# Kernel tuning notes

Measured on AMD Instinct MI355X. Metric: run time of the kernel, lower is better.

## Reference

```python
import jax, jax.numpy as jnp
import numpy as np
import math

SCALE = 30.0
MARGIN = 0.5
THRESH = -math.cos(MARGIN)          # easy_margin=False branch
SIN_M = math.sin(MARGIN)
OUT_INDICATOR = 1.0

B, D, C = 256, 512, 100000


def setup_inputs() -> dict:
    key = jax.random.key(0)
    k1, k2, k3 = jax.random.split(key, 3)
    feat = jax.random.normal(k1, (B, D), dtype=jnp.float32)
    # xavier_uniform_ for [C, D] weight
    bound = math.sqrt(6.0 / (C + D))
    weights = jax.random.uniform(k2, (C, D), dtype=jnp.float32, minval=-bound, maxval=bound)
    label = jax.random.randint(k3, (B,), 0, C, dtype=jnp.int64)
    return {"feat": feat, "weights": weights, "label": label}


def reference(feat, weights, label):
    # L2-normalize features and class weights, then cosine logits  [B, C]
    nf = feat / jnp.linalg.norm(feat, axis=-1, keepdims=True)
    nw = weights / jnp.linalg.norm(weights, axis=-1, keepdims=True)
    cos = jnp.matmul(nf, nw.T)

    rows = jnp.arange(feat.shape[0])
    cos_target = cos[rows, label]                     # [B] cos(theta_yi)
    cond = cos_target > THRESH

    # vectorized equivalent of the per-row scatter loop
    margin_tables = jnp.zeros_like(cos).at[rows, label].add(
        jnp.where(cond, MARGIN, 0.0).astype(cos.dtype))
    margin_tables_ext = jnp.zeros_like(cos).at[rows, label].add(
        jnp.where(cond, 0.0, -MARGIN * SIN_M).astype(cos.dtype))
    margin_tables_ext = margin_tables_ext * OUT_INDICATOR

    marginal_logits = SCALE * (jnp.cos(jnp.arccos(cos) + margin_tables) + margin_tables_ext)
    return marginal_logits, SCALE * cos, weights
```

## Files before the change

### kernel.cpp

```cpp
#include <hip/hip_runtime.h>
#include <math.h>
#include <stdint.h>

typedef __attribute__((ext_vector_type(8))) short short8;
typedef __attribute__((ext_vector_type(4))) float f32x4;
typedef __attribute__((ext_vector_type(4))) unsigned int u32x4;

#define SCALE   30.0f
#define MARGIN  0.5f
#define COS_M   0.8775825618903728f
#define SIN_M   0.4794255386042030f
#define THRESH  (-0.8775825618903728f)

constexpr int Bsz = 256;
constexpr int Dd  = 512;
constexpr int Cc  = 100000;
constexpr int NT  = 782;
constexpr int KT  = 16;
constexpr int TILE_EL   = 4096;
constexpr int COMP_TILE = KT * TILE_EL;

__device__ __forceinline__ unsigned short f2bf(float x) {
    unsigned int u = __float_as_uint(x);
    u += 0x7fffu + ((u >> 16) & 1u);
    return (unsigned short)(u >> 16);
}
__device__ __forceinline__ float bf2f(unsigned short h) {
    return __uint_as_float(((unsigned int)h) << 16);
}

#define GLL16(gptr, lptr)                                                              \
    __builtin_amdgcn_global_load_lds(                                                  \
        (const __attribute__((address_space(1))) unsigned int*)(gptr),                 \
        (__attribute__((address_space(3))) unsigned int*)(lptr), 16, 0, 0)

__device__ __forceinline__ int swz_off(int rr, int ch) {
    return rr * 32 + ((ch ^ ((rr >> 1) & 3)) * 8);
}

__device__ __forceinline__ void split2(float a, float b, unsigned int& hp, unsigned int& lp) {
    unsigned short h0 = f2bf(a), h1 = f2bf(b);
    unsigned short l0 = f2bf(a - bf2f(h0));
    unsigned short l1 = f2bf(b - bf2f(h1));
    hp = (unsigned int)h0 | ((unsigned int)h1 << 16);
    lp = (unsigned int)l0 | ((unsigned int)l1 << 16);
}

__global__ __launch_bounds__(256) void prep_kernel(
    const float* __restrict__ W, const float* __restrict__ F,
    float* __restrict__ inv_w, float* __restrict__ w_copy,
    unsigned short* __restrict__ whM, unsigned short* __restrict__ wlM,
    unsigned short* __restrict__ whL, unsigned short* __restrict__ wlL,
    unsigned short* __restrict__ Ah,  unsigned short* __restrict__ Al)
{
    const int wid = threadIdx.x >> 6, lane = threadIdx.x & 63;
    const int tk = lane >> 2, ch = lane & 3;

    {
        int row = blockIdx.x * 4 + wid;
        const float* src = W + (size_t)row * Dd + lane * 8;
        f32x4 v0 = __builtin_nontemporal_load((const f32x4*)src);
        f32x4 v1 = __builtin_nontemporal_load((const f32x4*)src + 1);
        float v[8] = {v0.x, v0.y, v0.z, v0.w, v1.x, v1.y, v1.z, v1.w};

        float s = 0.f;
        #pragma unroll
        for (int p = 0; p < 8; ++p) s += v[p] * v[p];
        #pragma unroll
        for (int off = 32; off >= 1; off >>= 1) s += __shfl_xor(s, off, 64);
        if (lane == 0) inv_w[row] = 1.0f / sqrtf(s);

        if (w_copy) {
            f32x4* dst = (f32x4*)(w_copy + (size_t)row * Dd + lane * 8);
            __builtin_nontemporal_store(v0, dst);
            __builtin_nontemporal_store(v1, dst + 1);
        }

        unsigned int hp[4], lp[4];
        #pragma unroll
        for (int p = 0; p < 4; ++p) split2(v[2*p], v[2*p+1], hp[p], lp[p]);

        int tn = row >> 7, rr = row & 127;
        size_t off = (size_t)tk * TILE_EL + swz_off(rr, ch);
        unsigned short* ph = (tn == NT-1) ? whL : whM + (size_t)tn * COMP_TILE;
        unsigned short* pl = (tn == NT-1) ? wlL : wlM + (size_t)tn * COMP_TILE;
        *(u32x4*)(ph + off) = u32x4{hp[0], hp[1], hp[2], hp[3]};
        *(u32x4*)(pl + off) = u32x4{lp[0], lp[1], lp[2], lp[3]};
    }

    if (blockIdx.x < Bsz / 4) {
        int row = blockIdx.x * 4 + wid;
        const float* src = F + (size_t)row * Dd + lane * 8;
        f32x4 v0 = __builtin_nontemporal_load((const f32x4*)src);
        f32x4 v1 = __builtin_nontemporal_load((const f32x4*)src + 1);
        float v[8] = {v0.x, v0.y, v0.z, v0.w, v1.x, v1.y, v1.z, v1.w};

        float s = 0.f;
        #pragma unroll
        for (int p = 0; p < 8; ++p) s += v[p] * v[p];
        #pragma unroll
        for (int off = 32; off >= 1; off >>= 1) s += __shfl_xor(s, off, 64);
        float inv = 1.0f / sqrtf(s);

        unsigned int hp[4], lp[4];
        #pragma unroll
        for (int p = 0; p < 4; ++p) split2(v[2*p] * inv, v[2*p+1] * inv, hp[p], lp[p]);

        int tm = row >> 7, rr = row & 127;
        size_t off = ((size_t)(tm * KT + tk)) * TILE_EL + swz_off(rr, ch);
        *(u32x4*)(Ah + off) = u32x4{hp[0], hp[1], hp[2], hp[3]};
        *(u32x4*)(Al + off) = u32x4{lp[0], lp[1], lp[2], lp[3]};
    }
}

__global__ __launch_bounds__(256, 2) void gemm_kernel(
    const unsigned short* __restrict__ Ah, const unsigned short* __restrict__ Al,
    const unsigned short* __restrict__ WhM, const unsigned short* __restrict__ WlM,
    const unsigned short* __restrict__ WhL, const unsigned short* __restrict__ WlL,
    const float* __restrict__ inv_w, const int* __restrict__ label,
    float* __restrict__ out_ml, float* __restrict__ out_cos)
{
    __shared__ __align__(16) unsigned short Ash[TILE_EL];
    __shared__ __align__(16) unsigned short Asl[TILE_EL];
    __shared__ __align__(16) unsigned short Bsh[TILE_EL];
    __shared__ __align__(16) unsigned short Bsl[TILE_EL];

    int lin = blockIdx.x;
    int xcd = lin & 7, pos = lin >> 3;
    int swz = (xcd < 4 ? xcd * 196 : 784 + (xcd - 4) * 195) + pos;
    int tn = (NT - 1) - (swz >> 1);
    int tm = swz & 1;

    const int tid  = threadIdx.x;
    const int wid  = tid >> 6, lane = tid & 63;
    const int wm   = wid >> 1, wn   = wid & 1;
    const int lr   = lane & 15, lc  = lane >> 4;

    const unsigned short* ah0 = Ah + (size_t)tm * COMP_TILE;
    const unsigned short* al0 = Al + (size_t)tm * COMP_TILE;
    const unsigned short* bh0 = (tn == NT-1) ? WhL : WhM + (size_t)tn * COMP_TILE;
    const unsigned short* bl0 = (tn == NT-1) ? WlL : WlM + (size_t)tn * COMP_TILE;

    f32x4 acc[4][4];
    #pragma unroll
    for (int i = 0; i < 4; ++i)
        #pragma unroll
        for (int j = 0; j < 4; ++j)
            acc[i][j] = f32x4{0.f, 0.f, 0.f, 0.f};

    int aoff[4], boff[4];
    #pragma unroll
    for (int i = 0; i < 4; ++i) {
        aoff[i] = swz_off(wm * 64 + i * 16 + lr, lc);
        boff[i] = swz_off(wn * 64 + i * 16 + lr, lc);
    }

    for (int tk = 0; tk < KT; ++tk) {
        const unsigned short* ga  = ah0 + tk * TILE_EL;
        const unsigned short* gal = al0 + tk * TILE_EL;
        const unsigned short* gb  = bh0 + tk * TILE_EL;
        const unsigned short* gbl = bl0 + tk * TILE_EL;
        __syncthreads();
        GLL16(ga  + tid * 8,        &Ash[tid * 8]);
        GLL16(ga  + 2048 + tid * 8, &Ash[2048 + tid * 8]);
        GLL16(gal + tid * 8,        &Asl[tid * 8]);
        GLL16(gal + 2048 + tid * 8, &Asl[2048 + tid * 8]);
        GLL16(gb  + tid * 8,        &Bsh[tid * 8]);
        GLL16(gb  + 2048 + tid * 8, &Bsh[2048 + tid * 8]);
        GLL16(gbl + tid * 8,        &Bsl[tid * 8]);
        GLL16(gbl + 2048 + tid * 8, &Bsl[2048 + tid * 8]);
        __syncthreads();

        short8 fah[4], fal[4], fbh[4], fbl[4];
        #pragma unroll
        for (int i = 0; i < 4; ++i) {
            fah[i] = *(const short8*)&Ash[aoff[i]];
            fal[i] = *(const short8*)&Asl[aoff[i]];
            fbh[i] = *(const short8*)&Bsh[boff[i]];
            fbl[i] = *(const short8*)&Bsl[boff[i]];
        }
        #pragma unroll
        for (int i = 0; i < 4; ++i)
            #pragma unroll
            for (int j = 0; j < 4; ++j) {
                acc[i][j] = __builtin_amdgcn_mfma_f32_16x16x32_bf16(fah[i], fbh[j], acc[i][j], 0, 0, 0);
                acc[i][j] = __builtin_amdgcn_mfma_f32_16x16x32_bf16(fah[i], fbl[j], acc[i][j], 0, 0, 0);
                acc[i][j] = __builtin_amdgcn_mfma_f32_16x16x32_bf16(fal[i], fbh[j], acc[i][j], 0, 0, 0);
            }
    }

    const int n0  = tn * 128 + wn * 64;
    const int m0g = tm * 128 + wm * 64;
    float invw[4]; int ncol[4]; bool nok[4];
    #pragma unroll
    for (int j = 0; j < 4; ++j) {
        ncol[j] = n0 + j * 16 + lr;
        nok[j]  = (ncol[j] < Cc);
        invw[j] = nok[j] ? inv_w[ncol[j]] : 0.0f;
    }
    #pragma unroll
    for (int i = 0; i < 4; ++i) {
        #pragma unroll
        for (int r = 0; r < 4; ++r) {
            int m = m0g + i * 16 + lc * 4 + r;
            int lab = label[m];
            size_t base = (size_t)m * Cc;
            #pragma unroll
            for (int j = 0; j < 4; ++j) {
                float cosv = acc[i][j][r] * invw[j];
                float sc = SCALE * cosv;
                float ml = sc;
                if (ncol[j] == lab) {
                    if (cosv > THRESH) {
                        float sint = sqrtf(fmaxf(0.f, 1.f - cosv * cosv));
                        ml = SCALE * (cosv * COS_M - sint * SIN_M);
                    } else {
                        ml = SCALE * (cosv - MARGIN * SIN_M);
                    }
                }
                if (nok[j]) {
                    __builtin_nontemporal_store(ml, out_ml  + base + ncol[j]);
                    __builtin_nontemporal_store(sc, out_cos + base + ncol[j]);
                }
            }
        }
    }
}

extern "C" void kernel_launch(void* const* d_in, const int* in_sizes, int n_in,
                              void* d_out, int out_size, void* d_ws, size_t ws_size,
                              hipStream_t stream) {
    const float* feat  = (const float*)d_in[0];
    const float* W     = (const float*)d_in[1];
    const int*   label = (const int*)d_in[2];

    float* out     = (float*)d_out;
    float* out_ml  = out;
    float* out_cos = out + (size_t)Bsz * Cc;
    float* out_w   = out + (size_t)2 * Bsz * Cc;

    char* ws = (char*)d_ws;
    float* inv_w = (float*)ws;
    size_t off = (size_t)Cc * 4;
    unsigned short* Ah = (unsigned short*)(ws + off); off += (size_t)2 * COMP_TILE * 2;
    unsigned short* Al = (unsigned short*)(ws + off); off += (size_t)2 * COMP_TILE * 2;

    const size_t wsplit_bytes = (size_t)2 * NT * COMP_TILE * 2;
    bool big = ws_size >= off + wsplit_bytes;

    unsigned short *whM, *wlM, *whL, *wlL;
    float* w_copy;
    if (big) {
        whM = (unsigned short*)(ws + off);
        wlM = whM + (size_t)NT * COMP_TILE;
        whL = whM + (size_t)(NT - 1) * COMP_TILE;
        wlL = wlM + (size_t)(NT - 1) * COMP_TILE;
        w_copy = out_w;
    } else {
        whM = (unsigned short*)out_w;
        wlM = whM + (size_t)(NT - 1) * COMP_TILE;
        whL = (unsigned short*)(ws + off); off += (size_t)COMP_TILE * 2;
        wlL = (unsigned short*)(ws + off); off += (size_t)COMP_TILE * 2;
        w_copy = nullptr;
    }

    hipLaunchKernelGGL(prep_kernel, dim3(Cc / 4), dim3(256), 0, stream,
                       W, feat, inv_w, w_copy, whM, wlM, whL, wlL, Ah, Al);
    hipLaunchKernelGGL(gemm_kernel, dim3(2 * NT), dim3(256), 0, stream,
                       Ah, Al, whM, wlM, whL, wlL, inv_w, label, out_ml, out_cos);
    if (!big) {
        hipMemcpyAsync(out_w, W, (size_t)Cc * Dd * sizeof(float),
                       hipMemcpyDeviceToDevice, stream);
    }
}
```

Baseline: 628.8 us.

## Double-buffer LDS tiles to overlap global loads with MFMA compute

```diff
diff --git a/kernel.cpp b/kernel.cpp
--- a/kernel.cpp
+++ b/kernel.cpp
@@ -120,10 +120,10 @@
     const float* __restrict__ inv_w, const int* __restrict__ label,
     float* __restrict__ out_ml, float* __restrict__ out_cos)
 {
-    __shared__ __align__(16) unsigned short Ash[TILE_EL];
-    __shared__ __align__(16) unsigned short Asl[TILE_EL];
-    __shared__ __align__(16) unsigned short Bsh[TILE_EL];
-    __shared__ __align__(16) unsigned short Bsl[TILE_EL];
+    __shared__ __align__(16) unsigned short Ash[2][TILE_EL];
+    __shared__ __align__(16) unsigned short Asl[2][TILE_EL];
+    __shared__ __align__(16) unsigned short Bsh[2][TILE_EL];
+    __shared__ __align__(16) unsigned short Bsl[2][TILE_EL];
 
     int lin = blockIdx.x;
     int xcd = lin & 7, pos = lin >> 3;
@@ -155,29 +155,36 @@
         boff[i] = swz_off(wn * 64 + i * 16 + lr, lc);
     }
 
+    #define STAGE(c, t)                                                                \
+        do {                                                                           \
+            const unsigned short* ga_  = ah0 + (t) * TILE_EL;                          \
+            const unsigned short* gal_ = al0 + (t) * TILE_EL;                          \
+            const unsigned short* gb_  = bh0 + (t) * TILE_EL;                          \
+            const unsigned short* gbl_ = bl0 + (t) * TILE_EL;                          \
+            GLL16(ga_  + tid * 8,        &Ash[c][tid * 8]);                            \
+            GLL16(ga_  + 2048 + tid * 8, &Ash[c][2048 + tid * 8]);                     \
+            GLL16(gal_ + tid * 8,        &Asl[c][tid * 8]);                            \
+            GLL16(gal_ + 2048 + tid * 8, &Asl[c][2048 + tid * 8]);                     \
+            GLL16(gb_  + tid * 8,        &Bsh[c][tid * 8]);                            \
+            GLL16(gb_  + 2048 + tid * 8, &Bsh[c][2048 + tid * 8]);                     \
+            GLL16(gbl_ + tid * 8,        &Bsl[c][tid * 8]);                            \
+            GLL16(gbl_ + 2048 + tid * 8, &Bsl[c][2048 + tid * 8]);                     \
+        } while (0)
+
+    STAGE(0, 0);
+    __syncthreads();
+
+    int cur = 0;
     for (int tk = 0; tk < KT; ++tk) {
-        const unsigned short* ga  = ah0 + tk * TILE_EL;
-        const unsigned short* gal = al0 + tk * TILE_EL;
-        const unsigned short* gb  = bh0 + tk * TILE_EL;
-        const unsigned short* gbl = bl0 + tk * TILE_EL;
-        __syncthreads();
-        GLL16(ga  + tid * 8,        &Ash[tid * 8]);
-        GLL16(ga  + 2048 + tid * 8, &Ash[2048 + tid * 8]);
-        GLL16(gal + tid * 8,        &Asl[tid * 8]);
-        GLL16(gal + 2048 + tid * 8, &Asl[2048 + tid * 8]);
-        GLL16(gb  + tid * 8,        &Bsh[tid * 8]);
-        GLL16(gb  + 2048 + tid * 8, &Bsh[2048 + tid * 8]);
-        GLL16(gbl + tid * 8,        &Bsl[tid * 8]);
-        GLL16(gbl + 2048 + tid * 8, &Bsl[2048 + tid * 8]);
-        __syncthreads();
+        if (tk + 1 < KT) STAGE(cur ^ 1, tk + 1);
 
         short8 fah[4], fal[4], fbh[4], fbl[4];
         #pragma unroll
         for (int i = 0; i < 4; ++i) {
-            fah[i] = *(const short8*)&Ash[aoff[i]];
-            fal[i] = *(const short8*)&Asl[aoff[i]];
-            fbh[i] = *(const short8*)&Bsh[boff[i]];
-            fbl[i] = *(const short8*)&Bsl[boff[i]];
+            fah[i] = *(const short8*)&Ash[cur][aoff[i]];
+            fal[i] = *(const short8*)&Asl[cur][aoff[i]];
+            fbh[i] = *(const short8*)&Bsh[cur][boff[i]];
+            fbl[i] = *(const short8*)&Bsl[cur][boff[i]];
         }
         #pragma unroll
         for (int i = 0; i < 4; ++i)
@@ -187,7 +194,11 @@
                 acc[i][j] = __builtin_amdgcn_mfma_f32_16x16x32_bf16(fah[i], fbl[j], acc[i][j], 0, 0, 0);
                 acc[i][j] = __builtin_amdgcn_mfma_f32_16x16x32_bf16(fal[i], fbh[j], acc[i][j], 0, 0, 0);
             }
-    }
+
+        __syncthreads();
+        cur ^= 1;
+    }
+    #undef STAGE
 
     const int n0  = tn * 128 + wn * 64;
     const int m0g = tm * 128 + wm * 64;
```

After: 675.8 us. 7.5% more time.
